# Performance work log

Measured on AMD Instinct MI355X. Metric: run time of the kernel, lower is better.

Reference implementation:

```python
import jax, jax.numpy as jnp
import numpy as np

B, T, GH, GW, C = 4, 8, 20, 36, 512
HEADS = 4
HD_HEAD = C // HEADS
WS = (5, 9)
EXP = (2, 4)
HD = 1960
OUT = (60, 108)
KS, ST, PD = (7, 7), (3, 3), (3, 3)
SCALE = HD_HEAD ** -0.5
NV = GH * GW  # fold positions per frame = 720


def _valid_ind_rolled():
    wh, ww = WS
    e0, e1 = EXP
    masks = []
    for s0, s1 in ((slice(0, wh - e0), slice(0, ww - e1)),
                   (slice(0, wh - e0), slice(e1, None)),
                   (slice(e0, None), slice(0, ww - e1)),
                   (slice(e0, None), slice(e1, None))):
        m = np.ones((wh, ww), np.float32)
        m[s0, s1] = 0
        masks.append(m)
    return np.nonzero(np.stack(masks, 0).reshape(-1))[0]

VALID_ROLLED = _valid_ind_rolled()  # 120 valid rolled positions


def layernorm(x, g, b, eps=1e-5):
    m = x.mean(-1, keepdims=True)
    v = ((x - m) ** 2).mean(-1, keepdims=True)
    return (x - m) * jax.lax.rsqrt(v + eps) * g + b


def win_part(t):
    # (B,T,H,W,C) -> (nW*B, T, wh*ww, C)
    Bb, Tt, Hh, Ww, Cc = t.shape
    wh, ww = WS
    t = t.reshape(Bb, Tt, Hh // wh, wh, Ww // ww, ww, Cc)
    return t.transpose(0, 2, 4, 1, 3, 5, 6).reshape(-1, Tt, wh * ww, Cc)


def split_heads(t):
    # (nWB,T,n,C) -> (nWB, heads, T*n, hd)
    nWB, Tt, n, Cc = t.shape
    return t.reshape(nWB, Tt, n, HEADS, HD_HEAD).transpose(0, 3, 1, 2, 4).reshape(nWB, HEADS, Tt * n, HD_HEAD)


def win_rev(w, Bb):
    # (nWB, T*wh*ww, C) -> (B,T,H,W,C)
    wh, ww = WS
    w = w.reshape(Bb, GH // wh, GW // ww, T, wh, ww, -1)
    return w.transpose(0, 3, 1, 4, 2, 5, 6).reshape(Bb, T, GH, GW, -1)


def _unfold(x):
    # x: (N,C,H,W) -> (N, C*kh*kw, L), torch F.unfold ordering (C outer)
    N, Cc, Hs, Wsz = x.shape
    kh, kw = KS; sh, sw = ST; ph, pw = PD
    oh = (Hs + 2 * ph - kh) // sh + 1
    ow = (Wsz + 2 * pw - kw) // sw + 1
    xp = jnp.pad(x, ((0, 0), (0, 0), (ph, ph), (pw, pw)))
    R = np.arange(kh)[:, None] + np.arange(oh)[None, :] * sh
    Cl = np.arange(kw)[:, None] + np.arange(ow)[None, :] * sw
    p = xp[:, :, R[:, None, :, None], Cl[None, :, None, :]]  # (N,C,kh,kw,oh,ow)
    return p.reshape(N, Cc * kh * kw, oh * ow)


def _fold(cols, Hs, Wsz):
    # cols: (N, C*kh*kw, L) -> (N, C, Hs, Wsz), overlap-add (torch F.fold)
    N = cols.shape[0]
    kh, kw = KS; sh, sw = ST; ph, pw = PD
    oh = (Hs + 2 * ph - kh) // sh + 1
    ow = (Wsz + 2 * pw - kw) // sw + 1
    Cc = cols.shape[1] // (kh * kw)
    vals = cols.reshape(N, Cc, kh, kw, oh, ow)
    R = np.arange(kh)[:, None] + np.arange(oh)[None, :] * sh
    Cl = np.arange(kw)[:, None] + np.arange(ow)[None, :] * sw
    out = jnp.zeros((N, Cc, Hs + 2 * ph, Wsz + 2 * pw), cols.dtype)
    out = out.at[:, :, R[:, None, :, None], Cl[None, :, None, :]].add(vals)
    return out[:, :, ph:ph + Hs, pw:pw + Wsz]


def _dwconv(x, w, b, pad):
    # depthwise conv, x: (N,Cin,H,W), w: (Cin,1,kh,kw)
    y = jax.lax.conv_general_dilated(x, w, (1, 1), [(pad, pad), (pad, pad)],
                                     dimension_numbers=('NCHW', 'OIHW', 'NCHW'),
                                     feature_group_count=x.shape[1])
    return y + b[None, :, None, None]


def _attention(x, w_qkv, b_qkv, w_proj, b_proj):
    Bb = x.shape[0]
    qkv = x @ w_qkv + b_qkv
    q, k, v = jnp.split(qkv, 3, axis=-1)
    q_w = split_heads(win_part(q))  # (nWB, heads, T*45, hd)
    k_w = split_heads(win_part(k))
    v_w = split_heads(win_part(v))
    e0, e1 = EXP
    shifts = ((-e0, -e1), (-e0, e1), (e0, -e1), (e0, e1))

    def rolled(t):
        parts = [win_part(jnp.roll(t, (s0, s1), axis=(2, 3))) for s0, s1 in shifts]
        r = jnp.concatenate(parts, axis=2)  # (nWB, T, 4*wh*ww, C)
        nWB = r.shape[0]
        r = r.reshape(nWB, T, 4 * WS[0] * WS[1], HEADS, HD_HEAD).transpose(0, 3, 1, 2, 4)
        r = r[:, :, :, VALID_ROLLED]  # (nWB, heads, T, 120, hd)
        return r.reshape(nWB, HEADS, -1, HD_HEAD)

    k_all = jnp.concatenate([k_w, rolled(k)], axis=2)  # (nWB, heads, T*165, hd)
    v_all = jnp.concatenate([v_w, rolled(v)], axis=2)
    attn = jnp.einsum('whqd,whkd->whqk', q_w * SCALE, k_all)
    attn = jax.nn.softmax(attn, axis=-1)
    out = jnp.einsum('whqk,whkd->whqd', attn, v_all)
    nWB = out.shape[0]
    out = out.transpose(0, 2, 1, 3).reshape(nWB, -1, C)
    out = out @ w_proj + b_proj
    return win_rev(out, Bb)


def _ffn(tok, w_fc1, b_fc1, w_c3, b_c3, w_c5, b_c5, w_fc2, b_fc2):
    # tok: (B, T*GH*GW, C)
    x = tok @ w_fc1 + b_fc1  # (B, n, HD)
    b, n, c = x.shape
    cols = x.reshape(-1, NV, c).transpose(0, 2, 1)  # (B*T, HD, NV)
    folded = _fold(cols, OUT[0], OUT[1])  # (B*T, HD//49, 60, 108)
    ones = jnp.ones((cols.shape[0], KS[0] * KS[1], NV), x.dtype)
    norm = _fold(ones, OUT[0], OUT[1])  # (B*T, 1, 60, 108) overlap counts
    x = _unfold(folded / norm).transpose(0, 2, 1).reshape(b, n, c)
    x = x.reshape(b * T, GH, GW, c).transpose(0, 3, 1, 2)  # (B*T, HD, GH, GW)
    x1, x2 = jnp.split(x, 2, axis=1)
    x = jnp.concatenate([_dwconv(x1, w_c3, b_c3, 1), _dwconv(x2, w_c5, b_c5, 2)], axis=1)
    x = x.transpose(0, 2, 3, 1).reshape(b, n, c)
    x = jax.nn.gelu(x, approximate=False)
    return x @ w_fc2 + b_fc2


def setup_inputs() -> dict:
    key = jax.random.key(0)
    ks = jax.random.split(key, 10)

    def nrm(k, shape, s=0.02):
        return jax.random.normal(k, shape, jnp.float32) * s

    return dict(
        x=jax.random.normal(ks[0], (B, T, GH, GW, C), jnp.float32),
        ln1_g=jnp.ones((C,), jnp.float32), ln1_b=jnp.zeros((C,), jnp.float32),
        ln2_g=jnp.ones((C,), jnp.float32), ln2_b=jnp.zeros((C,), jnp.float32),
        w_qkv=nrm(ks[1], (C, 3 * C)), b_qkv=jnp.zeros((3 * C,), jnp.float32),
        w_proj=nrm(ks[2], (C, C)), b_proj=jnp.zeros((C,), jnp.float32),
        w_fc1=nrm(ks[3], (C, HD)), b_fc1=jnp.zeros((HD,), jnp.float32),
        w_c3=nrm(ks[4], (HD // 2, 1, 3, 3)), b_c3=jnp.zeros((HD // 2,), jnp.float32),
        w_c5=nrm(ks[5], (HD - HD // 2, 1, 5, 5)), b_c5=jnp.zeros((HD - HD // 2,), jnp.float32),
        w_fc2=nrm(ks[6], (HD, C)), b_fc2=jnp.zeros((C,), jnp.float32),
    )


def reference(x, ln1_g, ln1_b, ln2_g, ln2_b, w_qkv, b_qkv, w_proj, b_proj,
              w_fc1, b_fc1, w_c3, b_c3, w_c5, b_c5, w_fc2, b_fc2):
    shortcut = x
    att = _attention(layernorm(x, ln1_g, ln1_b), w_qkv, b_qkv, w_proj, b_proj)
    x = shortcut + att
    tok = x.reshape(B, T * GH * GW, C)
    tok = tok + _ffn(layernorm(tok, ln2_g, ln2_b), w_fc1, b_fc1, w_c3, b_c3, w_c5, b_c5, w_fc2, b_fc2)
    return tok.reshape(B, T, GH, GW, C)
```

## Files before the change

kernel.cpp:

```cpp
#include <hip/hip_runtime.h>
#include <hip/hip_bf16.h>
#include <math.h>

typedef __attribute__((ext_vector_type(8))) short short8;
typedef __attribute__((ext_vector_type(4))) float f32x4;

#define MFMA16(a,b,c) __builtin_amdgcn_mfma_f32_16x16x32_bf16((a),(b),(c),0,0,0)

__device__ __forceinline__ short f2bf(float f) {
  unsigned u = __builtin_bit_cast(unsigned, f);
  u += 0x7fffu + ((u >> 16) & 1u);
  return (short)(u >> 16);
}
__device__ __forceinline__ float bf2f(short s) {
  unsigned u = ((unsigned)(unsigned short)s) << 16;
  return __builtin_bit_cast(float, u);
}

#define SCALE_F 0.08838834764831845f

__device__ const int VR_TAB[120] = {
  5,6,7,8,14,15,16,17,23,24,25,26,27,28,29,30,31,32,33,34,35,36,37,38,39,40,41,42,43,44,
  45,46,47,48,54,55,56,57,63,64,65,66,72,73,74,75,76,77,78,79,80,81,82,83,84,85,86,87,88,89,
  90,91,92,93,94,95,96,97,98,99,100,101,102,103,104,105,106,107,113,114,115,116,122,123,124,125,131,132,133,134,
  135,136,137,138,139,140,141,142,143,144,145,146,147,148,149,150,151,152,153,154,155,156,162,163,164,165,171,172,173,174
};

__global__ __launch_bounds__(256) void wtrans_kernel(const float* __restrict__ w,
                                                     short* __restrict__ wt, int K, int N) {
  int idx = blockIdx.x * 256 + threadIdx.x;
  if (idx >= K * N) return;
  int k = idx / N, n = idx - k * N;
  wt[(size_t)n * K + k] = f2bf(w[idx]);
}

__global__ __launch_bounds__(256) void ln_kernel(const float* __restrict__ x,
                                                 const float* __restrict__ g,
                                                 const float* __restrict__ be,
                                                 short* __restrict__ out) {
  typedef __attribute__((ext_vector_type(4))) float fx4;
  int row = blockIdx.x * 4 + (threadIdx.x >> 6);
  int lane = threadIdx.x & 63;
  const float* xr = x + (size_t)row * 512 + lane * 8;
  fx4 a = *(const fx4*)xr;
  fx4 c = *(const fx4*)(xr + 4);
  float s = a[0]+a[1]+a[2]+a[3]+c[0]+c[1]+c[2]+c[3];
  float ss = a[0]*a[0]+a[1]*a[1]+a[2]*a[2]+a[3]*a[3]+c[0]*c[0]+c[1]*c[1]+c[2]*c[2]+c[3]*c[3];
  for (int off = 1; off < 64; off <<= 1) {
    s  += __shfl_xor(s, off);
    ss += __shfl_xor(ss, off);
  }
  float mean = s * (1.0f/512.0f);
  float var  = ss * (1.0f/512.0f) - mean*mean;
  float rstd = rsqrtf(var + 1e-5f);
  const float* gp = g + lane*8;
  const float* bp = be + lane*8;
  short8 o;
  #pragma unroll
  for (int j = 0; j < 4; ++j) o[j]   = f2bf((a[j]-mean)*rstd*gp[j]   + bp[j]);
  #pragma unroll
  for (int j = 0; j < 4; ++j) o[4+j] = f2bf((c[j]-mean)*rstd*gp[4+j] + bp[4+j]);
  *(short8*)(out + (size_t)row * 512 + lane * 8) = o;
}

template<int OUT_BF16, int RESID, int LAYOUT>
__global__ __launch_bounds__(256) void gemm_kernel(
    const short* __restrict__ A, const short* __restrict__ Bt,
    const float* __restrict__ bias, const float* __restrict__ resid,
    void* __restrict__ outp, int N, int K) {
  const int m0 = blockIdx.x * 128, n0 = blockIdx.y * 128;
  const int tid = threadIdx.x;
  const int wave = tid >> 6, lane = tid & 63, lg = lane >> 4, lc = lane & 15;
  const int wr = wave >> 1, wc = wave & 1;
  __shared__ short As[128][40];
  __shared__ short Bs[128][40];
  f32x4 acc[4][4];
  #pragma unroll
  for (int i = 0; i < 4; ++i)
    #pragma unroll
    for (int j = 0; j < 4; ++j) { acc[i][j][0]=0.f; acc[i][j][1]=0.f; acc[i][j][2]=0.f; acc[i][j][3]=0.f; }
  const int steps = (K + 31) >> 5;
  for (int kt = 0; kt < steps; ++kt) {
    const int k0 = kt << 5;
    __syncthreads();
    #pragma unroll
    for (int it = 0; it < 2; ++it) {
      int row = (tid >> 2) + (it << 6);
      int kk = k0 + (tid & 3) * 8;
      short8 av = {0,0,0,0,0,0,0,0};
      short8 bv = {0,0,0,0,0,0,0,0};
      if (kk + 8 <= K) {
        av = *(const short8*)(A + (size_t)(m0 + row) * K + kk);
        int nrow = n0 + row;
        if (nrow < N) bv = *(const short8*)(Bt + (size_t)nrow * K + kk);
      }
      *(short8*)&As[row][(tid & 3) * 8] = av;
      *(short8*)&Bs[row][(tid & 3) * 8] = bv;
    }
    __syncthreads();
    short8 af[4], bfv[4];
    #pragma unroll
    for (int i = 0; i < 4; ++i) af[i]  = *(const short8*)&As[wr*64 + i*16 + lc][lg*8];
    #pragma unroll
    for (int j = 0; j < 4; ++j) bfv[j] = *(const short8*)&Bs[wc*64 + j*16 + lc][lg*8];
    #pragma unroll
    for (int i = 0; i < 4; ++i)
      #pragma unroll
      for (int j = 0; j < 4; ++j)
        acc[i][j] = MFMA16(af[i], bfv[j], acc[i][j]);
  }
  #pragma unroll
  for (int j = 0; j < 4; ++j) {
    int col = n0 + wc*64 + j*16 + lc;
    if (col >= N) continue;
    float bb = bias[col];
    #pragma unroll
    for (int i = 0; i < 4; ++i) {
      #pragma unroll
      for (int r = 0; r < 4; ++r) {
        int rowg = m0 + wr*64 + i*16 + lg*4 + r;
        float v = acc[i][j][r] + bb;
        if (RESID) v += resid[(size_t)rowg * N + col];
        if (LAYOUT == 1) {
          int nn = rowg / 720, sp = rowg - nn*720;
          ((short*)outp)[(size_t)nn*1411200 + (size_t)col*720 + sp] = f2bf(v);
        } else if (OUT_BF16) {
          ((short*)outp)[(size_t)rowg * N + col] = f2bf(v);
        } else {
          ((float*)outp)[(size_t)rowg * N + col] = v;
        }
      }
    }
  }
}

__global__ __launch_bounds__(256) void attn_kernel(const short* __restrict__ qkv,
                                                   short* __restrict__ aout) {
  const int qb = blockIdx.x, h = blockIdx.y, win = blockIdx.z;
  const int b = win >> 4, hb = (win >> 2) & 3, wb = win & 3;
  const int tid = threadIdx.x;
  const int wave = tid >> 6, lane = tid & 63, lg = lane >> 4, lc = lane & 15;

  __shared__ short Kc[64][136];
  __shared__ short Vt[128][72];
  __shared__ short Pl[4][16][40];

  int qa = qb*64 + wave*16 + lc; if (qa > 359) qa = 359;
  int tq = qa / 45, pq = qa - tq * 45;
  int mq = ((b*8 + tq)*20 + hb*5 + pq/9)*36 + wb*9 + (pq%9);
  const short* qptr = qkv + (size_t)mq * 1536 + h*128 + lg*8;
  short8 a_q[4];
  #pragma unroll
  for (int ks = 0; ks < 4; ++ks) a_q[ks] = *(const short8*)(qptr + ks*32);

  float m_run[4], l_run[4];
  f32x4 o_acc[8];
  #pragma unroll
  for (int i = 0; i < 4; ++i) { m_run[i] = -INFINITY; l_run[i] = 0.f; }
  #pragma unroll
  for (int dt = 0; dt < 8; ++dt) { o_acc[dt][0]=0.f; o_acc[dt][1]=0.f; o_acc[dt][2]=0.f; o_acc[dt][3]=0.f; }

  const int kl = tid >> 2, qpart = tid & 3;

  for (int c0 = 0; c0 < 21; ++c0) {
    int n = c0*64 + kl;
    bool valid = (n < 1320);
    int mk = 0;
    if (valid) {
      int t, gh, gw;
      if (n < 360) {
        t = n / 45; int p = n - t*45;
        gh = hb*5 + p/9; gw = wb*9 + (p%9);
      } else {
        int n2 = n - 360; t = n2 / 120; int vi = n2 - t*120;
        int f = VR_TAB[vi]; int s = f / 45; int p = f - s*45;
        int r = p / 9, cc = p - r*9;
        int sh0 = (s < 2) ? -2 : 2;
        int sh1 = (s & 1) ? 4 : -4;
        gh = (hb*5 + r - sh0 + 20) % 20;
        gw = (wb*9 + cc - sh1 + 36) % 36;
      }
      mk = ((b*8 + t)*20 + gh)*36 + gw;
    }
    const short* kp = qkv + (size_t)mk * 1536 + 512 + h*128 + qpart*32;
    #pragma unroll
    for (int u = 0; u < 4; ++u) {
      short8 kv = {0,0,0,0,0,0,0,0};
      short8 vv = {0,0,0,0,0,0,0,0};
      if (valid) {
        kv = *(const short8*)(kp + u*8);
        vv = *(const short8*)(kp + 512 + u*8);
      }
      int d0 = qpart*32 + u*8;
      *(short8*)&Kc[kl][d0] = kv;
      #pragma unroll
      for (int jj = 0; jj < 8; ++jj) Vt[d0 + jj][kl] = vv[jj];
    }
    __syncthreads();

    #pragma unroll
    for (int kt2 = 0; kt2 < 2; ++kt2) {
      const int kb = kt2 * 32;
      f32x4 s0, s1;
      s0[0]=0.f;s0[1]=0.f;s0[2]=0.f;s0[3]=0.f;
      s1[0]=0.f;s1[1]=0.f;s1[2]=0.f;s1[3]=0.f;
      #pragma unroll
      for (int ks = 0; ks < 4; ++ks) {
        short8 b0 = *(const short8*)&Kc[kb + lc][ks*32 + lg*8];
        short8 b1 = *(const short8*)&Kc[kb + 16 + lc][ks*32 + lg*8];
        s0 = MFMA16(a_q[ks], b0, s0);
        s1 = MFMA16(a_q[ks], b1, s1);
      }
      int key0 = c0*64 + kb + lc;
      bool v0k = key0 < 1320, v1k = (key0 + 16) < 1320;
      float p0[4], p1[4], fs[4];
      #pragma unroll
      for (int i = 0; i < 4; ++i) {
        float a0 = v0k ? s0[i] * SCALE_F : -1e30f;
        float a1 = v1k ? s1[i] * SCALE_F : -1e30f;
        float tm = fmaxf(a0, a1);
        for (int off = 1; off < 16; off <<= 1) tm = fmaxf(tm, __shfl_xor(tm, off));
        float mn = fmaxf(m_run[i], tm);
        float f = __expf(m_run[i] - mn);
        p0[i] = __expf(a0 - mn);
        p1[i] = __expf(a1 - mn);
        float ps = p0[i] + p1[i];
        for (int off = 1; off < 16; off <<= 1) ps += __shfl_xor(ps, off);
        l_run[i] = l_run[i] * f + ps;
        m_run[i] = mn;
        fs[i] = f;
      }
      #pragma unroll
      for (int dt = 0; dt < 8; ++dt)
        #pragma unroll
        for (int i = 0; i < 4; ++i) o_acc[dt][i] *= fs[i];
      #pragma unroll
      for (int i = 0; i < 4; ++i) {
        Pl[wave][4*lg + i][lc]      = f2bf(p0[i]);
        Pl[wave][4*lg + i][16 + lc] = f2bf(p1[i]);
      }
      __syncthreads();
      short8 pa = *(const short8*)&Pl[wave][lc][lg*8];
      #pragma unroll
      for (int dt = 0; dt < 8; ++dt) {
        short8 bv = *(const short8*)&Vt[dt*16 + lc][kb + lg*8];
        o_acc[dt] = MFMA16(pa, bv, o_acc[dt]);
      }
      __syncthreads();
    }
  }
  #pragma unroll
  for (int i = 0; i < 4; ++i) {
    int q = qb*64 + wave*16 + 4*lg + i;
    if (q >= 360) continue;
    float inv = 1.0f / l_run[i];
    int t = q / 45, p = q - t*45;
    int m = ((b*8 + t)*20 + hb*5 + p/9)*36 + wb*9 + (p%9);
    short* op = aout + (size_t)m * 512 + h*128 + lc;
    #pragma unroll
    for (int dt = 0; dt < 8; ++dt) op[dt*16] = f2bf(o_acc[dt][i] * inv);
  }
}

__global__ __launch_bounds__(256) void smooth_kernel(const short* __restrict__ h1t,
                                                     float* __restrict__ sm) {
  const int c40 = blockIdx.x, n = blockIdx.y;
  const int tid = threadIdx.x;
  const short* slab = h1t + (size_t)n*1411200 + (size_t)c40*49*720;
  float* outp = sm + (size_t)(n*40 + c40) * 6480;
  for (int p = tid; p < 6480; p += 256) {
    int y = p / 108, x = p - y*108;
    int y3 = y/3, ym = y - 3*y3;
    int x3 = x/3, xm = x - 3*x3;
    int jlo = (y3 == 19) ? 1 : 0, jhi = (y3 == 0) ? 1 : 2;
    int ilo = (x3 == 35) ? 1 : 0, ihi = (x3 == 0) ? 1 : 2;
    float s = 0.f;
    for (int j = jlo; j <= jhi; ++j) {
      int kh = ym + 3*j, oy = y3 + 1 - j;
      for (int i = ilo; i <= ihi; ++i) {
        int kw = xm + 3*i, ox = x3 + 1 - i;
        s += bf2f(slab[(kh*7 + kw)*720 + oy*36 + ox]);
      }
    }
    float cnt = (float)((jhi-jlo+1)*(ihi-ilo+1));
    outp[p] = s * (1.0f/cnt);
  }
}

__global__ __launch_bounds__(256) void conv_gelu_kernel(
    const float* __restrict__ sm,
    const float* __restrict__ w3, const float* __restrict__ b3,
    const float* __restrict__ w5, const float* __restrict__ b5,
    short* __restrict__ h3) {
  const int c40 = blockIdx.x, n = blockIdx.y;
  const int tid = threadIdx.x;
  __shared__ float P[64*114];
  __shared__ float wl[1225];
  __shared__ float wb[49];
  #pragma unroll
  for (int i = 0; i < 8; ++i) {
    int i4 = i*256 + tid;
    if (i4 < 1824) ((f32x4*)P)[i4] = f32x4{0.f,0.f,0.f,0.f};
  }
  const bool is3 = (c40 < 20);
  {
    const int W = is3 ? 9 : 25;
    const float* wsrc = is3 ? (w3 + c40*441) : (w5 + (size_t)(c40-20)*1225);
    for (int i = tid; i < 49*W; i += 256) wl[i] = wsrc[i];
    if (tid < 49) wb[tid] = is3 ? b3[c40*49 + tid] : b5[(c40-20)*49 + tid];
  }
  __syncthreads();
  const float* smp = sm + (size_t)(n*40 + c40) * 6480;
  for (int i = tid; i < 6480; i += 256) {
    int Y = i / 108, X = i - Y*108;
    P[(Y+3)*114 + X+3] = smp[i];
  }
  __syncthreads();

  for (int tt = tid; tt < 980; tt += 256) {
    int gh = tt / 49, k = tt - gh*49;
    int kh = k / 7, kw = k - kh*7;
    size_t obase = ((size_t)(n*720 + gh*36))*1960 + c40*49 + k;
    float bias = wb[k];
    if (is3) {
      float wr_[3][3];
      #pragma unroll
      for (int r = 0; r < 3; ++r)
        #pragma unroll
        for (int c = 0; c < 3; ++c) wr_[r][c] = wl[k*9 + r*3 + c];
      int rb[3];
      #pragma unroll
      for (int r = 0; r < 3; ++r) {
        int iy = gh + r - 1;
        int Y = 3*iy + kh - 3;
        rb[r] = ((unsigned)iy < 20u) ? (Y+3)*114 : 0;
      }
      float win[3][3];
      #pragma unroll
      for (int c = 0; c < 2; ++c) {
        int ix = c - 1;
        int X3 = 3*ix + kw;
        int xo = ((unsigned)ix < 36u) ? X3 : 0;
        #pragma unroll
        for (int r = 0; r < 3; ++r) win[r][c] = P[rb[r] + xo];
      }
      #pragma unroll
      for (int gw = 0; gw < 36; ++gw) {
        {
          int ix = gw + 1;
          int X3 = 3*ix + kw;
          int xo = ((unsigned)ix < 36u) ? X3 : 0;
          const int slot = (gw+2)%3;
          #pragma unroll
          for (int r = 0; r < 3; ++r) win[r][slot] = P[rb[r] + xo];
        }
        float acc = bias;
        #pragma unroll
        for (int r = 0; r < 3; ++r)
          #pragma unroll
          for (int c = 0; c < 3; ++c) acc += wr_[r][c] * win[r][(gw+c)%3];
        float g = 0.5f*acc*(1.f+erff(acc*0.70710678118654752f));
        h3[obase + (size_t)gw*1960] = f2bf(g);
      }
    } else {
      float wr_[5][5];
      #pragma unroll
      for (int r = 0; r < 5; ++r)
        #pragma unroll
        for (int c = 0; c < 5; ++c) wr_[r][c] = wl[k*25 + r*5 + c];
      int rb[5];
      #pragma unroll
      for (int r = 0; r < 5; ++r) {
        int iy = gh + r - 2;
        int Y = 3*iy + kh - 3;
        rb[r] = ((unsigned)iy < 20u) ? (Y+3)*114 : 0;
      }
      float win[5][5];
      #pragma unroll
      for (int c = 0; c < 4; ++c) {
        int ix = c - 2;
        int X3 = 3*ix + kw;
        int xo = ((unsigned)ix < 36u) ? X3 : 0;
        #pragma unroll
        for (int r = 0; r < 5; ++r) win[r][c] = P[rb[r] + xo];
      }
      #pragma unroll
      for (int gw = 0; gw < 36; ++gw) {
        {
          int ix = gw + 2;
          int X3 = 3*ix + kw;
          int xo = ((unsigned)ix < 36u) ? X3 : 0;
          const int slot = (gw+4)%5;
          #pragma unroll
          for (int r = 0; r < 5; ++r) win[r][slot] = P[rb[r] + xo];
        }
        float acc = bias;
        #pragma unroll
        for (int r = 0; r < 5; ++r)
          #pragma unroll
          for (int c = 0; c < 5; ++c) acc += wr_[r][c] * win[r][(gw+c)%5];
        float g = 0.5f*acc*(1.f+erff(acc*0.70710678118654752f));
        h3[obase + (size_t)gw*1960] = f2bf(g);
      }
    }
  }
}

extern "C" void kernel_launch(void* const* d_in, const int* in_sizes, int n_in,
                              void* d_out, int out_size, void* d_ws, size_t ws_size,
                              hipStream_t stream) {
  const float* x      = (const float*)d_in[0];
  const float* ln1_g  = (const float*)d_in[1];
  const float* ln1_b  = (const float*)d_in[2];
  const float* ln2_g  = (const float*)d_in[3];
  const float* ln2_b  = (const float*)d_in[4];
  const float* w_qkv  = (const float*)d_in[5];
  const float* b_qkv  = (const float*)d_in[6];
  const float* w_proj = (const float*)d_in[7];
  const float* b_proj = (const float*)d_in[8];
  const float* w_fc1  = (const float*)d_in[9];
  const float* b_fc1  = (const float*)d_in[10];
  const float* w_c3   = (const float*)d_in[11];
  const float* b_c3   = (const float*)d_in[12];
  const float* w_c5   = (const float*)d_in[13];
  const float* b_c5   = (const float*)d_in[14];
  const float* w_fc2  = (const float*)d_in[15];
  const float* b_fc2  = (const float*)d_in[16];

  char* ws = (char*)d_ws;
  short* wqkvT  = (short*)(ws + 0);
  short* wprojT = (short*)(ws + 1572864);
  short* wfc1T  = (short*)(ws + 2097152);
  short* wfc2T  = (short*)(ws + 4104192);
  short* lnb    = (short*)(ws + 6111232);
  short* bigb   = (short*)(ws + 29704192);
  short* attnb  = (short*)(ws + 120020992);
  float* x2     = (float*)(ws + 143613952);
  float* smooth = (float*)(ws + 190799872);

  wtrans_kernel<<<(512*1536 + 255)/256, 256, 0, stream>>>(w_qkv, wqkvT, 512, 1536);
  wtrans_kernel<<<(512*512  + 255)/256, 256, 0, stream>>>(w_proj, wprojT, 512, 512);
  wtrans_kernel<<<(512*1960 + 255)/256, 256, 0, stream>>>(w_fc1, wfc1T, 512, 1960);
  wtrans_kernel<<<(1960*512 + 255)/256, 256, 0, stream>>>(w_fc2, wfc2T, 1960, 512);

  ln_kernel<<<5760, 256, 0, stream>>>(x, ln1_g, ln1_b, lnb);
  gemm_kernel<1,0,0><<<dim3(180,12), 256, 0, stream>>>(lnb, wqkvT, b_qkv, nullptr, bigb, 1536, 512);
  attn_kernel<<<dim3(6,4,64), 256, 0, stream>>>(bigb, attnb);
  gemm_kernel<0,1,0><<<dim3(180,4), 256, 0, stream>>>(attnb, wprojT, b_proj, x, x2, 512, 512);

  ln_kernel<<<5760, 256, 0, stream>>>(x2, ln2_g, ln2_b, lnb);
  gemm_kernel<1,0,1><<<dim3(180,16), 256, 0, stream>>>(lnb, wfc1T, b_fc1, nullptr, bigb, 1960, 512);
  smooth_kernel<<<dim3(40,32), 256, 0, stream>>>(bigb, smooth);
  conv_gelu_kernel<<<dim3(40,32), 256, 0, stream>>>(smooth, w_c3, b_c3, w_c5, b_c5, bigb);
  gemm_kernel<0,1,0><<<dim3(180,4), 256, 0, stream>>>(bigb, wfc2T, b_fc2, x2, (float*)d_out, 512, 1960);
}
```

Measured before the change: 1.045 ms.

## Compute transposed attention scores, keep P in registers, swizzle V tile

The attention kernel now computes S^T (keys × queries) with MFMA, so each lane holds scores for one query across the key dimension. That lets the online softmax run on a 64-key chunk per step with only two cross-lane shuffles. The P matrix is repacked into MFMA A-operand fragments through lane shuffles instead of being staged in a shared-memory buffer, which removes two __syncthreads per 32-key step. The transposed V tile in LDS is XOR-swizzled to reduce bank conflicts on the transpose writes and fragment reads. In exchange the code adds more shuffle traffic and more intricate index logic.

```diff
diff --git a/kernel.cpp b/kernel.cpp
--- a/kernel.cpp
+++ b/kernel.cpp
@@ -4,6 +4,7 @@
 
 typedef __attribute__((ext_vector_type(8))) short short8;
 typedef __attribute__((ext_vector_type(4))) float f32x4;
+typedef __attribute__((ext_vector_type(4))) int int4v;
 
 #define MFMA16(a,b,c) __builtin_amdgcn_mfma_f32_16x16x32_bf16((a),(b),(c),0,0,0)
 
@@ -15,6 +16,9 @@
 __device__ __forceinline__ float bf2f(short s) {
   unsigned u = ((unsigned)(unsigned short)s) << 16;
   return __builtin_bit_cast(float, u);
+}
+__device__ __forceinline__ unsigned packbf(float lo, float hi) {
+  return (unsigned)(unsigned short)f2bf(lo) | ((unsigned)(unsigned short)f2bf(hi) << 16);
 }
 
 #define SCALE_F 0.08838834764831845f
@@ -143,20 +147,17 @@
 
   __shared__ short Kc[64][136];
   __shared__ short Vt[128][72];
-  __shared__ short Pl[4][16][40];
 
   int qa = qb*64 + wave*16 + lc; if (qa > 359) qa = 359;
   int tq = qa / 45, pq = qa - tq * 45;
   int mq = ((b*8 + tq)*20 + hb*5 + pq/9)*36 + wb*9 + (pq%9);
   const short* qptr = qkv + (size_t)mq * 1536 + h*128 + lg*8;
-  short8 a_q[4];
-  #pragma unroll
-  for (int ks = 0; ks < 4; ++ks) a_q[ks] = *(const short8*)(qptr + ks*32);
-
-  float m_run[4], l_run[4];
+  short8 q_f[4];
+  #pragma unroll
+  for (int ks = 0; ks < 4; ++ks) q_f[ks] = *(const short8*)(qptr + ks*32);
+
+  float m_run = -INFINITY, l_run = 0.f;
   f32x4 o_acc[8];
-  #pragma unroll
-  for (int i = 0; i < 4; ++i) { m_run[i] = -INFINITY; l_run[i] = 0.f; }
   #pragma unroll
   for (int dt = 0; dt < 8; ++dt) { o_acc[dt][0]=0.f; o_acc[dt][1]=0.f; o_acc[dt][2]=0.f; o_acc[dt][3]=0.f; }
 
@@ -193,72 +194,106 @@
       }
       int d0 = qpart*32 + u*8;
       *(short8*)&Kc[kl][d0] = kv;
-      #pragma unroll
-      for (int jj = 0; jj < 8; ++jj) Vt[d0 + jj][kl] = vv[jj];
+      int colb = (((kl>>3) ^ ((qpart<<1) | (u & 1))) << 3) | (kl & 7);
+      #pragma unroll
+      for (int jj = 0; jj < 8; ++jj) Vt[d0 + jj][colb] = vv[jj];
     }
     __syncthreads();
 
-    #pragma unroll
-    for (int kt2 = 0; kt2 < 2; ++kt2) {
-      const int kb = kt2 * 32;
-      f32x4 s0, s1;
-      s0[0]=0.f;s0[1]=0.f;s0[2]=0.f;s0[3]=0.f;
-      s1[0]=0.f;s1[1]=0.f;s1[2]=0.f;s1[3]=0.f;
+    f32x4 sv[4];
+    #pragma unroll
+    for (int t = 0; t < 4; ++t) { sv[t][0]=0.f; sv[t][1]=0.f; sv[t][2]=0.f; sv[t][3]=0.f; }
+    #pragma unroll
+    for (int t = 0; t < 4; ++t)
       #pragma unroll
       for (int ks = 0; ks < 4; ++ks) {
-        short8 b0 = *(const short8*)&Kc[kb + lc][ks*32 + lg*8];
-        short8 b1 = *(const short8*)&Kc[kb + 16 + lc][ks*32 + lg*8];
-        s0 = MFMA16(a_q[ks], b0, s0);
-        s1 = MFMA16(a_q[ks], b1, s1);
-      }
-      int key0 = c0*64 + kb + lc;
-      bool v0k = key0 < 1320, v1k = (key0 + 16) < 1320;
-      float p0[4], p1[4], fs[4];
-      #pragma unroll
-      for (int i = 0; i < 4; ++i) {
-        float a0 = v0k ? s0[i] * SCALE_F : -1e30f;
-        float a1 = v1k ? s1[i] * SCALE_F : -1e30f;
-        float tm = fmaxf(a0, a1);
-        for (int off = 1; off < 16; off <<= 1) tm = fmaxf(tm, __shfl_xor(tm, off));
-        float mn = fmaxf(m_run[i], tm);
-        float f = __expf(m_run[i] - mn);
-        p0[i] = __expf(a0 - mn);
-        p1[i] = __expf(a1 - mn);
-        float ps = p0[i] + p1[i];
-        for (int off = 1; off < 16; off <<= 1) ps += __shfl_xor(ps, off);
-        l_run[i] = l_run[i] * f + ps;
-        m_run[i] = mn;
-        fs[i] = f;
-      }
-      #pragma unroll
-      for (int dt = 0; dt < 8; ++dt)
-        #pragma unroll
-        for (int i = 0; i < 4; ++i) o_acc[dt][i] *= fs[i];
-      #pragma unroll
-      for (int i = 0; i < 4; ++i) {
-        Pl[wave][4*lg + i][lc]      = f2bf(p0[i]);
-        Pl[wave][4*lg + i][16 + lc] = f2bf(p1[i]);
-      }
-      __syncthreads();
-      short8 pa = *(const short8*)&Pl[wave][lc][lg*8];
-      #pragma unroll
-      for (int dt = 0; dt < 8; ++dt) {
-        short8 bv = *(const short8*)&Vt[dt*16 + lc][kb + lg*8];
-        o_acc[dt] = MFMA16(pa, bv, o_acc[dt]);
-      }
-      __syncthreads();
-    }
-  }
+        short8 kf = *(const short8*)&Kc[t*16 + lc][ks*32 + lg*8];
+        sv[t] = MFMA16(kf, q_f[ks], sv[t]);
+      }
+
+    if (c0 == 20) {
+      #pragma unroll
+      for (int t = 0; t < 4; ++t)
+        #pragma unroll
+        for (int r = 0; r < 4; ++r)
+          sv[t][r] = (t*16 + 4*lg + r < 40) ? sv[t][r]*SCALE_F : -1e30f;
+    } else {
+      #pragma unroll
+      for (int t = 0; t < 4; ++t)
+        #pragma unroll
+        for (int r = 0; r < 4; ++r) sv[t][r] *= SCALE_F;
+    }
+
+    float mc = -INFINITY;
+    #pragma unroll
+    for (int t = 0; t < 4; ++t)
+      #pragma unroll
+      for (int r = 0; r < 4; ++r) mc = fmaxf(mc, sv[t][r]);
+    mc = fmaxf(mc, __shfl_xor(mc, 16));
+    mc = fmaxf(mc, __shfl_xor(mc, 32));
+    float mn = fmaxf(m_run, mc);
+    float f = __expf(m_run - mn);
+    m_run = mn;
+    float ps = 0.f;
+    #pragma unroll
+    for (int t = 0; t < 4; ++t)
+      #pragma unroll
+      for (int r = 0; r < 4; ++r) { sv[t][r] = __expf(sv[t][r] - mn); ps += sv[t][r]; }
+    ps += __shfl_xor(ps, 16);
+    ps += __shfl_xor(ps, 32);
+    l_run = l_run * f + ps;
+
+    unsigned I[4][2];
+    #pragma unroll
+    for (int t = 0; t < 4; ++t) {
+      I[t][0] = packbf(sv[t][0], sv[t][1]);
+      I[t][1] = packbf(sv[t][2], sv[t][3]);
+    }
+    int4v pa0, pa1;
+    #pragma unroll
+    for (int t = 0; t < 4; ++t)
+      #pragma unroll
+      for (int w = 0; w < 2; ++w)
+        #pragma unroll
+        for (int X = 0; X < 2; ++X) {
+          int tmp = __shfl((int)I[t][w], ((lg & 1)*2 + X)*16 + lc);
+          int m = 2*X + w;
+          if ((lg >> 1) == (t & 1)) {
+            if (t < 2) pa0[m] = tmp; else pa1[m] = tmp;
+          }
+        }
+    short8 pa0s = __builtin_bit_cast(short8, pa0);
+    short8 pa1s = __builtin_bit_cast(short8, pa1);
+
+    float fr[4];
+    #pragma unroll
+    for (int r = 0; r < 4; ++r) fr[r] = __shfl(f, 4*lg + r);
+    #pragma unroll
+    for (int dt = 0; dt < 8; ++dt)
+      #pragma unroll
+      for (int r = 0; r < 4; ++r) o_acc[dt][r] *= fr[r];
+    #pragma unroll
+    for (int dt = 0; dt < 8; ++dt) {
+      int d = dt*16 + lc;
+      int swz = ((d >> 5) << 1) | ((d >> 3) & 1);
+      short8 bv0 = *(const short8*)&Vt[d][((0 + lg) ^ swz) << 3];
+      o_acc[dt] = MFMA16(pa0s, bv0, o_acc[dt]);
+      short8 bv1 = *(const short8*)&Vt[d][((4 + lg) ^ swz) << 3];
+      o_acc[dt] = MFMA16(pa1s, bv1, o_acc[dt]);
+    }
+    __syncthreads();
+  }
+
   #pragma unroll
   for (int i = 0; i < 4; ++i) {
     int q = qb*64 + wave*16 + 4*lg + i;
     if (q >= 360) continue;
-    float inv = 1.0f / l_run[i];
+    float linv = 1.0f / __shfl(l_run, 4*lg + i);
     int t = q / 45, p = q - t*45;
     int m = ((b*8 + t)*20 + hb*5 + p/9)*36 + wb*9 + (p%9);
     short* op = aout + (size_t)m * 512 + h*128 + lc;
     #pragma unroll
-    for (int dt = 0; dt < 8; ++dt) op[dt*16] = f2bf(o_acc[dt][i] * inv);
+    for (int dt = 0; dt < 8; ++dt) op[dt*16] = f2bf(o_acc[dt][i] * linv);
   }
 }
 
```

New measurement: 1.030 ms. Within noise of the previous version (-1.4%).
